# Kernel optimization log

Hardware: AMD Instinct MI355X
Metric: run time of the kernel (lower is better)

## Reference

```python
import jax, jax.numpy as jnp
import numpy as np
import math

B, S, T = 64, 512, 512
N, F_NODE, F_TRIP = 2000, 128, 128
D, H, GD = 512, 8, 64  # concat fusion: D == H*GD
SECONDS_PER_DAY = 3600.0 * 24.0


def cyclical_feat(t, mask):
    # t,[B,L]; mask,[B,L] -> [B,L,2]  (matches tf concat of sin/cos on axis 2)
    ang = 2.0 * math.pi * t / SECONDS_PER_DAY
    return jnp.stack([jnp.sin(ang) * mask, jnp.cos(ang) * mask], axis=-1)


def gat(x, adj, W, a_src, a_dst):
    # GAT-style AttentionAggregator, concat fusion + relu activation.
    # x:[N,F], adj:[N,N] (0/1), W:[H,F,G], a_src/a_dst:[H,G]
    h = jnp.einsum('nf,hfg->hng', x, W)                      # [H,N,G]
    es = jnp.einsum('hng,hg->hn', h, a_src)                  # [H,N]
    ed = jnp.einsum('hng,hg->hn', h, a_dst)                  # [H,N]
    e = jax.nn.leaky_relu(es[:, :, None] + ed[:, None, :], 0.2)  # [H,N,N]
    e = jnp.where(adj[None, :, :] > 0, e, -1e9)
    attn = jax.nn.softmax(e, axis=-1)                        # [H,N,N]
    out = jnp.einsum('hij,hjg->hig', attn, h)                # [H,N,G]
    out = jnp.transpose(out, (1, 0, 2)).reshape(x.shape[0], -1)  # [N,H*G]
    return jax.nn.relu(out)


def reconstruct_from_graph(graph_emb, index_array):
    # Vectorized equivalent of the TF TensorArray loop: indices are 1-based
    # with 0 = pad; valid entries are left-compacted, so masked gather == 
    # boolean_mask + gather + right-pad.
    valid = index_array > 0                                   # [B,S]
    idx = jnp.maximum(index_array - 1, 0)                     # [B,S]
    return jnp.where(valid[..., None], graph_emb[idx], 0.0)   # [B,S,D]


def setup_inputs() -> dict:
    key = jax.random.key(0)
    ks = jax.random.split(key, 13)
    region_batch = jax.random.normal(ks[0], (N, F_NODE), jnp.float32)
    trip_batch = jax.random.normal(ks[1], (B, T, F_TRIP), jnp.float32)
    len_r = jax.random.randint(ks[2], (B,), S // 2, S + 1)
    len_t = jax.random.randint(ks[3], (B,), T // 2, T + 1)
    region_mask = (jnp.arange(S)[None, :] < len_r[:, None]).astype(jnp.float32)
    trip_mask = (jnp.arange(T)[None, :] < len_t[:, None]).astype(jnp.float32)
    graph_mask = (jax.random.uniform(ks[4], (N, N)) < 0.02).astype(jnp.float32)
    graph_mask = jnp.maximum(graph_mask, jnp.eye(N, dtype=jnp.float32))  # self loops
    index_array = jax.random.randint(ks[5], (B, S), 1, N + 1).astype(jnp.int32)
    index_array = index_array * region_mask.astype(jnp.int32)  # 0 = pad (right side)
    arrive = jax.random.uniform(ks[6], (B, S), jnp.float32, 0.0, SECONDS_PER_DAY)
    depart = jax.random.uniform(ks[7], (B, T), jnp.float32, 0.0, SECONDS_PER_DAY)
    W_trip = jax.random.normal(ks[8], (F_TRIP, D), jnp.float32) * 0.05
    W_gat = jax.random.normal(ks[9], (H, F_NODE, GD), jnp.float32) * 0.05
    a_src = jax.random.normal(ks[10], (H, GD), jnp.float32) * 0.05
    a_dst = jax.random.normal(ks[11], (H, GD), jnp.float32) * 0.05
    W_time = jax.random.normal(ks[12], (2, D), jnp.float32) * 0.05
    b_time = jnp.zeros((D,), jnp.float32)
    return dict(region_batch=region_batch, trip_batch=trip_batch,
                trip_mask=trip_mask, region_mask=region_mask, graph_mask=graph_mask,
                arrive=arrive, depart=depart, index_array=index_array,
                W_trip=W_trip, W_gat=W_gat, a_src=a_src, a_dst=a_dst,
                W_time=W_time, b_time=b_time)


def reference(region_batch, trip_batch, trip_mask, region_mask, graph_mask,
              arrive, depart, index_array, W_trip, W_gat, a_src, a_dst,
              W_time, b_time):
    # FeatureExtractionLayer assumed Dense(no bias) + relu; dropout=0 (eval).
    trip_embeddings = jax.nn.relu(jnp.einsum('btf,fd->btd', trip_batch, W_trip))
    graph_embeddings = gat(region_batch, graph_mask, W_gat, a_src, a_dst)  # [N,D]
    region_embeddings = reconstruct_from_graph(graph_embeddings, index_array)
    arrive_feat = cyclical_feat(arrive, region_mask)   # [B,S,2]
    depart_feat = cyclical_feat(depart, trip_mask)     # [B,T,2]
    region_embeddings = region_embeddings + arrive_feat @ W_time + b_time
    trip_embeddings = trip_embeddings + depart_feat @ W_time + b_time
    return (region_embeddings, trip_embeddings)
```

## Files before the change

kernel.cpp:

```cpp
#include <hip/hip_runtime.h>
#include <hip/hip_bf16.h>

#define NB 2000
#define FN 128
#define DD 512
#define HH 8
#define GG 64
#define BB 64
#define SS 512
#define TT 512

__device__ __forceinline__ bool is_bf16(const void* graph_mask) {
    return (((const unsigned*)graph_mask)[0] & 0xFFFFu) == 0x3F80u;
}

template<bool BF>
__device__ __forceinline__ float ld(const void* p, long i) {
    if constexpr (BF) return __bfloat162float(((const __hip_bfloat16*)p)[i]);
    else              return ((const float*)p)[i];
}
template<bool BF>
__device__ __forceinline__ void st(void* p, long i, float v) {
    if constexpr (BF) ((__hip_bfloat16*)p)[i] = __float2bfloat16(v);
    else              ((float*)p)[i] = v;
}

template<bool BF>
__device__ __forceinline__ void ld4(const void* p, long i, float* o) {
    if constexpr (BF) {
        const unsigned short* q = (const unsigned short*)p + i;
        uint2 v = *reinterpret_cast<const uint2*>(q);
        o[0] = __uint_as_float((v.x & 0xFFFFu) << 16);
        o[1] = __uint_as_float((v.x >> 16) << 16);
        o[2] = __uint_as_float((v.y & 0xFFFFu) << 16);
        o[3] = __uint_as_float((v.y >> 16) << 16);
    } else {
        float4 a = *reinterpret_cast<const float4*>((const float*)p + i);
        o[0]=a.x; o[1]=a.y; o[2]=a.z; o[3]=a.w;
    }
}
template<bool BF>
__device__ __forceinline__ void ld8(const void* p, long i, float* o) {
    if constexpr (BF) {
        const unsigned short* q = (const unsigned short*)p + i;
        uint4 v = *reinterpret_cast<const uint4*>(q);
        unsigned a0 = v.x, a1 = v.y, a2 = v.z, a3 = v.w;
        o[0] = __uint_as_float((a0 & 0xFFFFu) << 16);
        o[1] = __uint_as_float((a0 >> 16) << 16);
        o[2] = __uint_as_float((a1 & 0xFFFFu) << 16);
        o[3] = __uint_as_float((a1 >> 16) << 16);
        o[4] = __uint_as_float((a2 & 0xFFFFu) << 16);
        o[5] = __uint_as_float((a2 >> 16) << 16);
        o[6] = __uint_as_float((a3 & 0xFFFFu) << 16);
        o[7] = __uint_as_float((a3 >> 16) << 16);
    } else {
        const float* q = (const float*)p + i;
        float4 a = *reinterpret_cast<const float4*>(q);
        float4 b = *reinterpret_cast<const float4*>(q + 4);
        o[0]=a.x; o[1]=a.y; o[2]=a.z; o[3]=a.w;
        o[4]=b.x; o[5]=b.y; o[6]=b.z; o[7]=b.w;
    }
}
__device__ __forceinline__ unsigned pack_bf2(float a, float b) {
    __hip_bfloat16 x = __float2bfloat16(a), y = __float2bfloat16(b);
    return (unsigned)*(unsigned short*)&x | ((unsigned)*(unsigned short*)&y << 16);
}
template<bool BF>
__device__ __forceinline__ void st4(void* p, long i, const float* v) {
    if constexpr (BF) {
        unsigned short* q = (unsigned short*)p + i;
        *reinterpret_cast<uint2*>(q) = make_uint2(pack_bf2(v[0], v[1]), pack_bf2(v[2], v[3]));
    } else {
        *reinterpret_cast<float4*>((float*)p + i) = make_float4(v[0],v[1],v[2],v[3]);
    }
}
template<bool BF>
__device__ __forceinline__ void st8(void* p, long i, const float* v) {
    if constexpr (BF) {
        unsigned short* q = (unsigned short*)p + i;
        *reinterpret_cast<uint4*>(q) = make_uint4(
            pack_bf2(v[0], v[1]), pack_bf2(v[2], v[3]),
            pack_bf2(v[4], v[5]), pack_bf2(v[6], v[7]));
    } else {
        float* q = (float*)p + i;
        *reinterpret_cast<float4*>(q)     = make_float4(v[0],v[1],v[2],v[3]);
        *reinterpret_cast<float4*>(q + 4) = make_float4(v[4],v[5],v[6],v[7]);
    }
}

#define NPB 8

template<bool BF>
__device__ __forceinline__ void gat_h_body(
    const void* __restrict__ x, const void* __restrict__ Wg,
    const void* __restrict__ a_src, const void* __restrict__ a_dst,
    float* __restrict__ h_ws, float* __restrict__ es_ws, float* __restrict__ ed_ws,
    float (*__restrict__ xs)[FN])
{
    int n0  = blockIdx.x * NPB;
    int tid = threadIdx.x;
    int hh  = tid >> 5, gp = tid & 31;
    int g0  = gp * 2;

    if constexpr (BF) {
        for (int idx = tid; idx < NPB * FN / 8; idx += 256) {
            float o[8];
            ld8<BF>(x, (long)n0 * FN + idx * 8, o);
#pragma unroll
            for (int j = 0; j < 8; ++j) ((float*)xs)[idx * 8 + j] = o[j];
        }
    } else {
        const float4* src = (const float4*)((const float*)x + (long)n0 * FN);
        for (int idx = tid; idx < NPB * FN / 4; idx += 256)
            ((float4*)xs)[idx] = src[idx];
    }
    __syncthreads();

    float v0[NPB], v1[NPB];
#pragma unroll
    for (int nn = 0; nn < NPB; ++nn) { v0[nn] = 0.f; v1[nn] = 0.f; }

    if constexpr (BF) {
        const unsigned* wp = (const unsigned*)((const unsigned short*)Wg + (long)hh * FN * GG);
#pragma unroll 4
        for (int f = 0; f < FN; ++f) {
            unsigned w = wp[f * 32 + gp];
            float wx = __uint_as_float((w & 0xFFFFu) << 16);
            float wy = __uint_as_float((w >> 16) << 16);
#pragma unroll
            for (int nn = 0; nn < NPB; ++nn) {
                float xf = xs[nn][f];
                v0[nn] = fmaf(xf, wx, v0[nn]);
                v1[nn] = fmaf(xf, wy, v1[nn]);
            }
        }
    } else {
        const float2* wp = (const float2*)((const float*)Wg + (long)hh * FN * GG);
#pragma unroll 4
        for (int f = 0; f < FN; ++f) {
            float2 w = wp[f * 32 + gp];
#pragma unroll
            for (int nn = 0; nn < NPB; ++nn) {
                float xf = xs[nn][f];
                v0[nn] = fmaf(xf, w.x, v0[nn]);
                v1[nn] = fmaf(xf, w.y, v1[nn]);
            }
        }
    }

    float as0 = ld<BF>(a_src, hh * GG + g0), as1 = ld<BF>(a_src, hh * GG + g0 + 1);
    float ad0 = ld<BF>(a_dst, hh * GG + g0), ad1 = ld<BF>(a_dst, hh * GG + g0 + 1);
#pragma unroll
    for (int nn = 0; nn < NPB; ++nn) {
        int n = n0 + nn;
        *reinterpret_cast<float2*>(&h_ws[((long)hh * NB + n) * GG + g0]) =
            make_float2(v0[nn], v1[nn]);
        float s1 = v0[nn] * as0 + v1[nn] * as1;
        float s2 = v0[nn] * ad0 + v1[nn] * ad1;
        for (int off = 16; off > 0; off >>= 1) {
            s1 += __shfl_xor(s1, off);
            s2 += __shfl_xor(s2, off);
        }
        if (gp == 0) { es_ws[hh * NB + n] = s1; ed_ws[hh * NB + n] = s2; }
    }
}

__global__ __launch_bounds__(256) void gat_h_kernel(
    const void* x, const void* Wg, const void* a_src, const void* a_dst,
    float* h_ws, float* es_ws, float* ed_ws, const void* graph_mask)
{
    __shared__ float xs[NPB][FN];
    if (is_bf16(graph_mask)) gat_h_body<true >(x, Wg, a_src, a_dst, h_ws, es_ws, ed_ws, xs);
    else                     gat_h_body<false>(x, Wg, a_src, a_dst, h_ws, es_ws, ed_ws, xs);
}

#define ACAP 192

template<bool BF>
__device__ __forceinline__ void gat_attn_body(
    const void* __restrict__ adj,
    const float* __restrict__ h_ws, const float* __restrict__ es_ws,
    const float* __restrict__ ed_ws, float* __restrict__ ge_ws,
    int* __restrict__ jl, float (*__restrict__ wts)[ACAP],
    float* __restrict__ es_i, int* __restrict__ cnt)
{
    const int i    = blockIdx.x;
    const int tid  = threadIdx.x;
    const int w    = tid >> 6;
    const int lane = tid & 63;

    if (tid == 0) *cnt = 0;
    if (tid < HH) es_i[tid] = es_ws[tid * NB + i];
    __syncthreads();

    for (int base = w * 64; base < NB; base += 512) {
        int  j     = base + lane;
        bool valid = (j < NB) && (ld<BF>(adj, (long)i * NB + j) > 0.f);
        unsigned long long mask = __ballot(valid);
        int nv = __popcll(mask);
        int bs = 0;
        if (lane == 0 && nv) bs = atomicAdd(cnt, nv);
        bs = __shfl(bs, 0);
        if (valid) {
            int slot = bs + __popcll(mask & ((1ULL << lane) - 1ULL));
            jl[slot] = j;
        }
    }
    __syncthreads();
    const int cn = min(*cnt, ACAP);

    const float es = es_i[w];
    float e_r[3];
    float m = -INFINITY;
#pragma unroll
    for (int s = 0; s < 3; ++s) {
        int k = lane + s * 64;
        float e = -INFINITY;
        if (k < cn) {
            float ev = es + ed_ws[(long)w * NB + jl[k]];
            e = ev > 0.f ? ev : 0.2f * ev;
        }
        e_r[s] = e;
        m = fmaxf(m, e);
    }
    for (int off = 32; off > 0; off >>= 1) m = fmaxf(m, __shfl_xor(m, off));
    float l = 0.f;
#pragma unroll
    for (int s = 0; s < 3; ++s) {
        int k = lane + s * 64;
        if (k < cn) {
            float p = __expf(e_r[s] - m);
            wts[w][k] = p;
            l += p;
        }
    }
    for (int off = 32; off > 0; off >>= 1) l += __shfl_xor(l, off);

    const float* hp = h_ws + (long)w * NB * GG + lane;
    float acc = 0.f;
    int k = 0;
    for (; k + 4 <= cn; k += 4) {
        float e0 = wts[w][k],   e1 = wts[w][k+1];
        float e2 = wts[w][k+2], e3 = wts[w][k+3];
        int   j0 = jl[k],   j1 = jl[k+1], j2 = jl[k+2], j3 = jl[k+3];
        float h0 = hp[(long)j0 * GG];
        float h1 = hp[(long)j1 * GG];
        float h2 = hp[(long)j2 * GG];
        float h3 = hp[(long)j3 * GG];
        acc = fmaf(e3, h3, fmaf(e2, h2, fmaf(e1, h1, fmaf(e0, h0, acc))));
    }
    for (; k < cn; ++k)
        acc = fmaf(wts[w][k], hp[(long)jl[k] * GG], acc);

    ge_ws[(long)i * DD + w * GG + lane] = fmaxf(acc / l, 0.f);
}

__global__ __launch_bounds__(512) void gat_attn_kernel(
    const void* adj, const float* h_ws, const float* es_ws,
    const float* ed_ws, float* ge_ws)
{
    __shared__ int   jl[2048];
    __shared__ float wts[HH][ACAP];
    __shared__ float es_i[HH];
    __shared__ int   cnt;
    if (is_bf16(adj)) gat_attn_body<true >(adj, h_ws, es_ws, ed_ws, ge_ws, jl, wts, es_i, &cnt);
    else              gat_attn_body<false>(adj, h_ws, es_ws, ed_ws, ge_ws, jl, wts, es_i, &cnt);
}

template<bool BF>
__device__ __forceinline__ void region_out_body(
    const int* __restrict__ index_array, const void* __restrict__ arrive,
    const void* __restrict__ region_mask,
    const void* __restrict__ W_time, const void* __restrict__ b_time,
    const float* __restrict__ ge_ws, void* __restrict__ out)
{
    int row  = blockIdx.x * 4 + (threadIdx.x >> 6);
    int lane = threadIdx.x & 63;
    int d0   = lane * 8;
    int idx  = index_array[row];
    float mask = ld<BF>(region_mask, row);
    float t    = ld<BF>(arrive, row);
    float ang  = 6.28318530717958647692f * t / 86400.f;
    float sa = sinf(ang) * mask, ca = cosf(ang) * mask;
    float g[8] = {0.f,0.f,0.f,0.f,0.f,0.f,0.f,0.f};
    if (idx > 0) {
        const float* gp = ge_ws + (long)(idx - 1) * DD + d0;
        float4 a = *reinterpret_cast<const float4*>(gp);
        float4 b = *reinterpret_cast<const float4*>(gp + 4);
        g[0]=a.x; g[1]=a.y; g[2]=a.z; g[3]=a.w;
        g[4]=b.x; g[5]=b.y; g[6]=b.z; g[7]=b.w;
    }
    float wt0[8], wt1[8], bt[8], o[8];
    ld8<BF>(W_time, d0, wt0);
    ld8<BF>(W_time, DD + d0, wt1);
    ld8<BF>(b_time, d0, bt);
#pragma unroll
    for (int j = 0; j < 8; ++j)
        o[j] = g[j] + sa * wt0[j] + ca * wt1[j] + bt[j];
    st8<BF>(out, (long)row * DD + d0, o);
}

__global__ __launch_bounds__(256) void region_out_kernel(
    const int* index_array, const void* arrive, const void* region_mask,
    const void* W_time, const void* b_time, const float* ge_ws, void* out,
    const void* graph_mask)
{
    if (is_bf16(graph_mask))
        region_out_body<true >(index_array, arrive, region_mask, W_time, b_time, ge_ws, out);
    else
        region_out_body<false>(index_array, arrive, region_mask, W_time, b_time, ge_ws, out);
}

#define TBM 64
#define TBN 256

template<bool BF>
__device__ __forceinline__ void trip_out_body(
    const void* __restrict__ trip_batch, const void* __restrict__ W_trip,
    const void* __restrict__ depart, const void* __restrict__ trip_mask,
    const void* __restrict__ W_time, const void* __restrict__ b_time,
    void* __restrict__ out,
    float (*__restrict__ xs)[FN], float* __restrict__ sa_s, float* __restrict__ ca_s)
{
    const int tid  = threadIdx.x;
    const int ch   = blockIdx.x & 1;
    const int row0 = (blockIdx.x >> 1) * TBM;

    if constexpr (BF) {
        for (int idx = tid; idx < TBM * FN / 8; idx += 512) {
            float o[8];
            ld8<BF>(trip_batch, (long)row0 * FN + idx * 8, o);
            float4* dst = (float4*)((float*)xs + idx * 8);
            dst[0] = make_float4(o[0], o[1], o[2], o[3]);
            dst[1] = make_float4(o[4], o[5], o[6], o[7]);
        }
    } else {
        const float4* src = (const float4*)((const float*)trip_batch + (long)row0 * FN);
        for (int idx = tid; idx < TBM * FN / 4; idx += 512)
            ((float4*)xs)[idx] = src[idx];
    }
    if (tid < TBM) {
        int   row  = row0 + tid;
        float mask = ld<BF>(trip_mask, row);
        float t    = ld<BF>(depart, row);
        float ang  = 6.28318530717958647692f * t / 86400.f;
        sa_s[tid] = sinf(ang) * mask;
        ca_s[tid] = cosf(ang) * mask;
    }
    __syncthreads();

    const int cg = tid & 63, rg = tid >> 6;
    const int c0 = ch * TBN + cg * 4;
    const int r0 = rg * 8;
    float acc[8][4];
#pragma unroll
    for (int i = 0; i < 8; ++i)
#pragma unroll
        for (int j = 0; j < 4; ++j) acc[i][j] = 0.f;

    float w0[4], w1[4], nw0[4], nw1[4];
    ld4<BF>(W_trip, 0L * DD + c0, w0);
    ld4<BF>(W_trip, 1L * DD + c0, w1);

    for (int k = 0; k < FN; k += 2) {
        if (k + 2 < FN) {
            ld4<BF>(W_trip, (long)(k + 2) * DD + c0, nw0);
            ld4<BF>(W_trip, (long)(k + 3) * DD + c0, nw1);
        }
        float2 xv[8];
#pragma unroll
        for (int i = 0; i < 8; ++i)
            xv[i] = *reinterpret_cast<const float2*>(&xs[r0 + i][k]);
#pragma unroll
        for (int i = 0; i < 8; ++i)
#pragma unroll
            for (int j = 0; j < 4; ++j)
                acc[i][j] = fmaf(xv[i].y, w1[j], fmaf(xv[i].x, w0[j], acc[i][j]));
        if (k + 2 < FN) {
#pragma unroll
            for (int j = 0; j < 4; ++j) { w0[j] = nw0[j]; w1[j] = nw1[j]; }
        }
    }

    float wt0[4], wt1[4], bt[4];
    ld4<BF>(W_time, c0, wt0);
    ld4<BF>(W_time, DD + c0, wt1);
    ld4<BF>(b_time, c0, bt);
    const long obase = (long)BB * SS * DD + (long)row0 * DD;
#pragma unroll
    for (int i = 0; i < 8; ++i) {
        float sa = sa_s[r0 + i], ca = ca_s[r0 + i];
        float o[4];
#pragma unroll
        for (int j = 0; j < 4; ++j)
            o[j] = fmaxf(acc[i][j], 0.f) + sa * wt0[j] + ca * wt1[j] + bt[j];
        st4<BF>(out, obase + (long)(r0 + i) * DD + c0, o);
    }
}

__global__ __launch_bounds__(512) void trip_out_kernel(
    const void* trip_batch, const void* W_trip, const void* depart,
    const void* trip_mask, const void* W_time, const void* b_time, void* out,
    const void* graph_mask)
{
    __shared__ float xs[TBM][FN];
    __shared__ float sa_s[TBM], ca_s[TBM];
    if (is_bf16(graph_mask))
        trip_out_body<true >(trip_batch, W_trip, depart, trip_mask, W_time, b_time, out, xs, sa_s, ca_s);
    else
        trip_out_body<false>(trip_batch, W_trip, depart, trip_mask, W_time, b_time, out, xs, sa_s, ca_s);
}

extern "C" void kernel_launch(void* const* d_in, const int* in_sizes, int n_in,
                              void* d_out, int out_size, void* d_ws, size_t ws_size,
                              hipStream_t stream) {
    const void* region_batch = d_in[0];
    const void* trip_batch   = d_in[1];
    const void* trip_mask    = d_in[2];
    const void* region_mask  = d_in[3];
    const void* graph_mask   = d_in[4];
    const void* arrive       = d_in[5];
    const void* depart       = d_in[6];
    const int*  index_array  = (const int*)d_in[7];
    const void* W_trip       = d_in[8];
    const void* W_gat        = d_in[9];
    const void* a_src        = d_in[10];
    const void* a_dst        = d_in[11];
    const void* W_time       = d_in[12];
    const void* b_time       = d_in[13];

    float* h_ws  = (float*)d_ws;
    float* es_ws = h_ws  + HH * NB * GG;
    float* ed_ws = es_ws + HH * NB;
    float* ge_ws = ed_ws + HH * NB;

    gat_h_kernel<<<NB / NPB, 256, 0, stream>>>(region_batch, W_gat, a_src, a_dst,
                                               h_ws, es_ws, ed_ws, graph_mask);
    gat_attn_kernel<<<NB, 512, 0, stream>>>(graph_mask, h_ws, es_ws, ed_ws, ge_ws);
    region_out_kernel<<<BB * SS / 4, 256, 0, stream>>>(index_array, arrive, region_mask,
                                                       W_time, b_time, ge_ws, d_out, graph_mask);
    trip_out_kernel<<<(BB * TT / TBM) * (DD / TBN), 512, 0, stream>>>(
        trip_batch, W_trip, depart, trip_mask, W_time, b_time, d_out, graph_mask);
}
```

Baseline: 290.5 us.

## Use split-bf16 MFMA for trip embedding GEMM with swizzled LDS tiles

Replaces the scalar FP32 FMA trip GEMM with MFMA 16x16x32 bf16 instructions. Each operand is split into high and low bf16 parts and three MFMAs are summed to keep near-FP32 accuracy. Tiles become 64x64 with XOR-swizzled shared memory and 256 threads per block. The epilogue now writes scalar, per-lane strided stores instead of vector stores, which may hurt store coalescing. The W transpose into LDS is also done with scalar writes.

New measurement: 286.3 us. Within noise of the previous version (-1.5%).

```diff
diff --git a/kernel.cpp b/kernel.cpp
--- a/kernel.cpp
+++ b/kernel.cpp
@@ -66,15 +66,6 @@
     return (unsigned)*(unsigned short*)&x | ((unsigned)*(unsigned short*)&y << 16);
 }
 template<bool BF>
-__device__ __forceinline__ void st4(void* p, long i, const float* v) {
-    if constexpr (BF) {
-        unsigned short* q = (unsigned short*)p + i;
-        *reinterpret_cast<uint2*>(q) = make_uint2(pack_bf2(v[0], v[1]), pack_bf2(v[2], v[3]));
-    } else {
-        *reinterpret_cast<float4*>((float*)p + i) = make_float4(v[0],v[1],v[2],v[3]);
-    }
-}
-template<bool BF>
 __device__ __forceinline__ void st8(void* p, long i, const float* v) {
     if constexpr (BF) {
         unsigned short* q = (unsigned short*)p + i;
@@ -86,6 +77,14 @@
         *reinterpret_cast<float4*>(q)     = make_float4(v[0],v[1],v[2],v[3]);
         *reinterpret_cast<float4*>(q + 4) = make_float4(v[4],v[5],v[6],v[7]);
     }
+}
+
+__device__ __forceinline__ unsigned short f2bf(float v) {
+    __hip_bfloat16 h = __float2bfloat16(v);
+    return *reinterpret_cast<unsigned short*>(&h);
+}
+__device__ __forceinline__ float bf2f(unsigned short s) {
+    return __uint_as_float((unsigned)s << 16);
 }
 
 #define NPB 8
@@ -311,104 +310,147 @@
         region_out_body<false>(index_array, arrive, region_mask, W_time, b_time, ge_ws, out);
 }
 
-#define TBM 64
-#define TBN 256
-
-template<bool BF>
-__device__ __forceinline__ void trip_out_body(
+typedef __attribute__((ext_vector_type(8))) short bf16x8;
+typedef __attribute__((ext_vector_type(4))) float f32x4;
+
+#define MFMA_BF16 __builtin_amdgcn_mfma_f32_16x16x32_bf16
+
+template<bool BF>
+__device__ __forceinline__ void trip_mfma_body(
     const void* __restrict__ trip_batch, const void* __restrict__ W_trip,
     const void* __restrict__ depart, const void* __restrict__ trip_mask,
     const void* __restrict__ W_time, const void* __restrict__ b_time,
     void* __restrict__ out,
-    float (*__restrict__ xs)[FN], float* __restrict__ sa_s, float* __restrict__ ca_s)
+    short* __restrict__ Xh, short* __restrict__ Xl,
+    short* __restrict__ Wh, short* __restrict__ Wl)
 {
     const int tid  = threadIdx.x;
-    const int ch   = blockIdx.x & 1;
-    const int row0 = (blockIdx.x >> 1) * TBM;
-
-    if constexpr (BF) {
-        for (int idx = tid; idx < TBM * FN / 8; idx += 512) {
-            float o[8];
-            ld8<BF>(trip_batch, (long)row0 * FN + idx * 8, o);
-            float4* dst = (float4*)((float*)xs + idx * 8);
-            dst[0] = make_float4(o[0], o[1], o[2], o[3]);
-            dst[1] = make_float4(o[4], o[5], o[6], o[7]);
-        }
-    } else {
-        const float4* src = (const float4*)((const float*)trip_batch + (long)row0 * FN);
-        for (int idx = tid; idx < TBM * FN / 4; idx += 512)
-            ((float4*)xs)[idx] = src[idx];
-    }
-    if (tid < TBM) {
-        int   row  = row0 + tid;
+    const int lane = tid & 63;
+    const int wv   = tid >> 6;
+    const int bx   = blockIdx.x & 7;
+    const int by   = blockIdx.x >> 3;
+    const int row0 = by * 64;
+    const int c0   = bx * 64;
+
+    f32x4 acc0 = {0.f,0.f,0.f,0.f}, acc1 = {0.f,0.f,0.f,0.f};
+    f32x4 acc2 = {0.f,0.f,0.f,0.f}, acc3 = {0.f,0.f,0.f,0.f};
+
+    const int mr  = wv * 16 + (lane & 15);
+    const int nrb = lane & 15;
+    const int kl  = (lane >> 4) * 8;
+
+    for (int kh = 0; kh < 2; ++kh) {
+        if (kh) __syncthreads();
+
+        for (int q = tid; q < 1024; q += 256) {
+            int r  = q >> 4;
+            int k4 = (q & 15) * 4;
+            float v[4];
+            ld4<BF>(trip_batch, (long)(row0 + r) * FN + kh * 64 + k4, v);
+            int base = r * 64 + (k4 ^ ((r & 7) << 3));
+            ushort4 hs, ls;
+            hs.x = f2bf(v[0]); ls.x = f2bf(v[0] - bf2f(hs.x));
+            hs.y = f2bf(v[1]); ls.y = f2bf(v[1] - bf2f(hs.y));
+            hs.z = f2bf(v[2]); ls.z = f2bf(v[2] - bf2f(hs.z));
+            hs.w = f2bf(v[3]); ls.w = f2bf(v[3] - bf2f(hs.w));
+            *reinterpret_cast<ushort4*>(&Xh[base]) = hs;
+            *reinterpret_cast<ushort4*>(&Xl[base]) = ls;
+        }
+        for (int q = tid; q < 1024; q += 256) {
+            int k  = q >> 4;
+            int n0 = (q & 15) * 4;
+            float v[4];
+            ld4<BF>(W_trip, (long)(kh * 64 + k) * DD + c0 + n0, v);
+#pragma unroll
+            for (int j = 0; j < 4; ++j) {
+                int n   = n0 + j;
+                int idx = n * 64 + (k ^ ((n & 7) << 3));
+                unsigned short h = f2bf(v[j]);
+                Wh[idx] = (short)h;
+                Wl[idx] = (short)f2bf(v[j] - bf2f(h));
+            }
+        }
+        __syncthreads();
+
+#pragma unroll
+        for (int kc = 0; kc < 2; ++kc) {
+            int k0 = kc * 32 + kl;
+            int ax = mr * 64 + (k0 ^ ((mr & 7) << 3));
+            bf16x8 ah = *reinterpret_cast<const bf16x8*>(&Xh[ax]);
+            bf16x8 al = *reinterpret_cast<const bf16x8*>(&Xl[ax]);
+            {
+                int nr = 0 + nrb, wi = nr * 64 + (k0 ^ ((nr & 7) << 3));
+                bf16x8 bh = *reinterpret_cast<const bf16x8*>(&Wh[wi]);
+                bf16x8 bl = *reinterpret_cast<const bf16x8*>(&Wl[wi]);
+                acc0 = MFMA_BF16(ah, bh, acc0, 0, 0, 0);
+                acc0 = MFMA_BF16(al, bh, acc0, 0, 0, 0);
+                acc0 = MFMA_BF16(ah, bl, acc0, 0, 0, 0);
+            }
+            {
+                int nr = 16 + nrb, wi = nr * 64 + (k0 ^ ((nr & 7) << 3));
+                bf16x8 bh = *reinterpret_cast<const bf16x8*>(&Wh[wi]);
+                bf16x8 bl = *reinterpret_cast<const bf16x8*>(&Wl[wi]);
+                acc1 = MFMA_BF16(ah, bh, acc1, 0, 0, 0);
+                acc1 = MFMA_BF16(al, bh, acc1, 0, 0, 0);
+                acc1 = MFMA_BF16(ah, bl, acc1, 0, 0, 0);
+            }
+            {
+                int nr = 32 + nrb, wi = nr * 64 + (k0 ^ ((nr & 7) << 3));
+                bf16x8 bh = *reinterpret_cast<const bf16x8*>(&Wh[wi]);
+                bf16x8 bl = *reinterpret_cast<const bf16x8*>(&Wl[wi]);
+                acc2 = MFMA_BF16(ah, bh, acc2, 0, 0, 0);
+                acc2 = MFMA_BF16(al, bh, acc2, 0, 0, 0);
+                acc2 = MFMA_BF16(ah, bl, acc2, 0, 0, 0);
+            }
+            {
+                int nr = 48 + nrb, wi = nr * 64 + (k0 ^ ((nr & 7) << 3));
+                bf16x8 bh = *reinterpret_cast<const bf16x8*>(&Wh[wi]);
+                bf16x8 bl = *reinterpret_cast<const bf16x8*>(&Wl[wi]);
+                acc3 = MFMA_BF16(ah, bh, acc3, 0, 0, 0);
+                acc3 = MFMA_BF16(al, bh, acc3, 0, 0, 0);
+                acc3 = MFMA_BF16(ah, bl, acc3, 0, 0, 0);
+            }
+        }
+    }
+
+    const int rbase = row0 + wv * 16 + (lane >> 4) * 4;
+    float sa[4], ca[4];
+#pragma unroll
+    for (int r = 0; r < 4; ++r) {
+        int   row  = rbase + r;
         float mask = ld<BF>(trip_mask, row);
         float t    = ld<BF>(depart, row);
         float ang  = 6.28318530717958647692f * t / 86400.f;
-        sa_s[tid] = sinf(ang) * mask;
-        ca_s[tid] = cosf(ang) * mask;
-    }
-    __syncthreads();
-
-    const int cg = tid & 63, rg = tid >> 6;
-    const int c0 = ch * TBN + cg * 4;
-    const int r0 = rg * 8;
-    float acc[8][4];
-#pragma unroll
-    for (int i = 0; i < 8; ++i)
-#pragma unroll
-        for (int j = 0; j < 4; ++j) acc[i][j] = 0.f;
-
-    float w0[4], w1[4], nw0[4], nw1[4];
-    ld4<BF>(W_trip, 0L * DD + c0, w0);
-    ld4<BF>(W_trip, 1L * DD + c0, w1);
-
-    for (int k = 0; k < FN; k += 2) {
-        if (k + 2 < FN) {
-            ld4<BF>(W_trip, (long)(k + 2) * DD + c0, nw0);
-            ld4<BF>(W_trip, (long)(k + 3) * DD + c0, nw1);
-        }
-        float2 xv[8];
-#pragma unroll
-        for (int i = 0; i < 8; ++i)
-            xv[i] = *reinterpret_cast<const float2*>(&xs[r0 + i][k]);
-#pragma unroll
-        for (int i = 0; i < 8; ++i)
-#pragma unroll
-            for (int j = 0; j < 4; ++j)
-                acc[i][j] = fmaf(xv[i].y, w1[j], fmaf(xv[i].x, w0[j], acc[i][j]));
-        if (k + 2 < FN) {
-#pragma unroll
-            for (int j = 0; j < 4; ++j) { w0[j] = nw0[j]; w1[j] = nw1[j]; }
-        }
-    }
-
-    float wt0[4], wt1[4], bt[4];
-    ld4<BF>(W_time, c0, wt0);
-    ld4<BF>(W_time, DD + c0, wt1);
-    ld4<BF>(b_time, c0, bt);
-    const long obase = (long)BB * SS * DD + (long)row0 * DD;
-#pragma unroll
-    for (int i = 0; i < 8; ++i) {
-        float sa = sa_s[r0 + i], ca = ca_s[r0 + i];
-        float o[4];
-#pragma unroll
-        for (int j = 0; j < 4; ++j)
-            o[j] = fmaxf(acc[i][j], 0.f) + sa * wt0[j] + ca * wt1[j] + bt[j];
-        st4<BF>(out, obase + (long)(r0 + i) * DD + c0, o);
-    }
-}
-
-__global__ __launch_bounds__(512) void trip_out_kernel(
+        sa[r] = sinf(ang) * mask;
+        ca[r] = cosf(ang) * mask;
+    }
+    const long obase = (long)BB * SS * DD;
+#pragma unroll
+    for (int nt = 0; nt < 4; ++nt) {
+        int   c   = c0 + nt * 16 + (lane & 15);
+        float wt0 = ld<BF>(W_time, c);
+        float wt1 = ld<BF>(W_time, DD + c);
+        float bt  = ld<BF>(b_time, c);
+        f32x4 a = (nt == 0) ? acc0 : (nt == 1) ? acc1 : (nt == 2) ? acc2 : acc3;
+#pragma unroll
+        for (int r = 0; r < 4; ++r) {
+            float o = fmaxf(a[r], 0.f) + sa[r] * wt0 + ca[r] * wt1 + bt;
+            st<BF>(out, obase + (long)(rbase + r) * DD + c, o);
+        }
+    }
+}
+
+__global__ __launch_bounds__(256) void trip_out_kernel(
     const void* trip_batch, const void* W_trip, const void* depart,
     const void* trip_mask, const void* W_time, const void* b_time, void* out,
     const void* graph_mask)
 {
-    __shared__ float xs[TBM][FN];
-    __shared__ float sa_s[TBM], ca_s[TBM];
+    __shared__ short Xh[64 * 64], Xl[64 * 64];
+    __shared__ short Wh[64 * 64], Wl[64 * 64];
     if (is_bf16(graph_mask))
-        trip_out_body<true >(trip_batch, W_trip, depart, trip_mask, W_time, b_time, out, xs, sa_s, ca_s);
+        trip_mfma_body<true >(trip_batch, W_trip, depart, trip_mask, W_time, b_time, out, Xh, Xl, Wh, Wl);
     else
-        trip_out_body<false>(trip_batch, W_trip, depart, trip_mask, W_time, b_time, out, xs, sa_s, ca_s);
+        trip_mfma_body<false>(trip_batch, W_trip, depart, trip_mask, W_time, b_time, out, Xh, Xl, Wh, Wl);
 }
 
 extern "C" void kernel_launch(void* const* d_in, const int* in_sizes, int n_in,
@@ -439,6 +481,6 @@
     gat_attn_kernel<<<NB, 512, 0, stream>>>(graph_mask, h_ws, es_ws, ed_ws, ge_ws);
     region_out_kernel<<<BB * SS / 4, 256, 0, stream>>>(index_array, arrive, region_mask,
                                                        W_time, b_time, ge_ws, d_out, graph_mask);
-    trip_out_kernel<<<(BB * TT / TBM) * (DD / TBN), 512, 0, stream>>>(
+    trip_out_kernel<<<(BB * TT / 64) * (DD / 64), 256, 0, stream>>>(
         trip_batch, W_trip, depart, trip_mask, W_time, b_time, d_out, graph_mask);
 }
```
